# Performance work log

Measured on AMD Instinct MI355X. Metric: run time of the kernel, lower is better.

Reference implementation:

```python
import jax, jax.numpy as jnp
import numpy as np

NUM_HEADS = 16
ATTN_WINDOW = 128  # half-width; mask is |i-j| <= ATTN_WINDOW
EMBED_DIM = 1024


def setup_inputs() -> dict:
    key = jax.random.key(0)
    ks = jax.random.split(key, 9)
    B, S, D = 2, 2048, EMBED_DIM
    s = 1.0 / np.sqrt(D)
    inp = {
        "x": jax.random.normal(ks[0], (B, S, D), dtype=jnp.float32),
        "Wq": jax.random.normal(ks[1], (D, D), dtype=jnp.float32) * s,
        "bq": jnp.zeros((D,), dtype=jnp.float32),
        "Wk": jax.random.normal(ks[2], (D, D), dtype=jnp.float32) * s,
        "bk": jnp.zeros((D,), dtype=jnp.float32),
        "Wv": jax.random.normal(ks[3], (D, D), dtype=jnp.float32) * s,
        "bv": jnp.zeros((D,), dtype=jnp.float32),
        "Wo": jax.random.normal(ks[4], (D, D), dtype=jnp.float32) * s,
        "bo": jnp.zeros((D,), dtype=jnp.float32),
    }
    return inp


def reference(x, Wq, bq, Wk, bk, Wv, bv, Wo, bo):
    B, S, D = x.shape
    H = NUM_HEADS
    dh = D // H
    # projections (nn.Linear: x @ W^T + b)
    q = (x @ Wq.T + bq).reshape(B, S, H, dh).transpose(0, 2, 1, 3)  # [B,H,S,dh]
    k = (x @ Wk.T + bk).reshape(B, S, H, dh).transpose(0, 2, 1, 3)
    v = (x @ Wv.T + bv).reshape(B, S, H, dh).transpose(0, 2, 1, 3)
    scale = 1.0 / jnp.sqrt(jnp.asarray(dh, dtype=jnp.float32))
    scores = jnp.einsum("bhqd,bhkd->bhqk", q, k) * scale  # [B,H,S,S]
    # sliding-window band mask: allowed iff |i - j| <= ATTN_WINDOW
    idx = jnp.arange(S)
    band = jnp.abs(idx[:, None] - idx[None, :]) <= ATTN_WINDOW  # [S,S] bool
    scores = jnp.where(band[None, None], scores, -jnp.inf)
    attn = jax.nn.softmax(scores, axis=-1)  # each row has >=1 valid entry
    ctx = jnp.einsum("bhqk,bhkd->bhqd", attn, v)
    ctx = ctx.transpose(0, 2, 1, 3).reshape(B, S, D)
    out = ctx @ Wo.T + bo
    return out, attn
```

## Files before the change

kernel.cpp:

```cpp
#include <hip/hip_runtime.h>
#include <cstddef>

#define NB 2
#define NH 16
#define SQ 2048
#define DM 1024
#define DH 64
#define WN 128

using half8  = __attribute__((ext_vector_type(8))) _Float16;
using half4  = __attribute__((ext_vector_type(4))) _Float16;
using floatx4 = __attribute__((ext_vector_type(4))) float;

__device__ __forceinline__ void gl_lds16(const _Float16* g, _Float16* l) {
    __builtin_amdgcn_global_load_lds(
        (const __attribute__((address_space(1))) void*)g,
        (__attribute__((address_space(3))) void*)l, 16, 0, 0);
}

__global__ __launch_bounds__(256) void cvt1(const float* __restrict__ s,
                                            _Float16* __restrict__ d, int n8)
{
    int idx = blockIdx.x * 256 + threadIdx.x;
    if (idx < n8) {
        const float4 a = ((const float4*)s)[idx * 2];
        const float4 b = ((const float4*)s)[idx * 2 + 1];
        half8 h;
        h[0] = (_Float16)a.x; h[1] = (_Float16)a.y;
        h[2] = (_Float16)a.z; h[3] = (_Float16)a.w;
        h[4] = (_Float16)b.x; h[5] = (_Float16)b.y;
        h[6] = (_Float16)b.z; h[7] = (_Float16)b.w;
        ((half8*)d)[idx] = h;
    }
}

__global__ __launch_bounds__(256) void cvt4(
    const float* __restrict__ s0, const float* __restrict__ s1,
    const float* __restrict__ s2, const float* __restrict__ s3,
    _Float16* __restrict__ d0, _Float16* __restrict__ d1,
    _Float16* __restrict__ d2, _Float16* __restrict__ d3, int n8)
{
    const float* s = (blockIdx.y == 0) ? s0 : (blockIdx.y == 1) ? s1
                   : (blockIdx.y == 2) ? s2 : s3;
    _Float16*   d = (blockIdx.y == 0) ? d0 : (blockIdx.y == 1) ? d1
                   : (blockIdx.y == 2) ? d2 : d3;
    int idx = blockIdx.x * 256 + threadIdx.x;
    if (idx < n8) {
        const float4 a = ((const float4*)s)[idx * 2];
        const float4 b = ((const float4*)s)[idx * 2 + 1];
        half8 h;
        h[0] = (_Float16)a.x; h[1] = (_Float16)a.y;
        h[2] = (_Float16)a.z; h[3] = (_Float16)a.w;
        h[4] = (_Float16)b.x; h[5] = (_Float16)b.y;
        h[6] = (_Float16)b.z; h[7] = (_Float16)b.w;
        ((half8*)d)[idx] = h;
    }
}

template <int OUT_HALF>
__global__ __launch_bounds__(256) void gemm_h(
    const _Float16* __restrict__ A,
    const _Float16* __restrict__ W0, const _Float16* __restrict__ W1,
    const _Float16* __restrict__ W2,
    const float* __restrict__ b0, const float* __restrict__ b1,
    const float* __restrict__ b2,
    void* __restrict__ O0, void* __restrict__ O1, void* __restrict__ O2)
{
    constexpr int K = DM, N = DM, BK = 64;

    const _Float16* Wp = (blockIdx.z == 0) ? W0 : (blockIdx.z == 1) ? W1 : W2;
    const float*    bb = (blockIdx.z == 0) ? b0 : (blockIdx.z == 1) ? b1 : b2;
    void*           Op = (blockIdx.z == 0) ? O0 : (blockIdx.z == 1) ? O1 : O2;

    __shared__ _Float16 Asl[128 * BK];
    __shared__ _Float16 Bsl[128 * BK];

    const int tid  = threadIdx.x;
    const int lane = tid & 63;
    const int w    = tid >> 6;
    const int wm   = w & 1, wn = w >> 1;
    const int m0   = blockIdx.y * 128;
    const int n0   = blockIdx.x * 128;

    const int l8 = lane >> 3;
    const int lc = lane & 7;

    floatx4 acc[4][4];
#pragma unroll
    for (int t = 0; t < 4; ++t)
#pragma unroll
        for (int u = 0; u < 4; ++u) acc[t][u] = (floatx4){0.f, 0.f, 0.f, 0.f};

    for (int k0 = 0; k0 < K; k0 += BK) {
        __syncthreads();
#pragma unroll
        for (int i = 0; i < 4; ++i) {
            const int r  = w * 8 + l8 + i * 32;
            const int ca = lc ^ (r & 7);
            gl_lds16(A  + (size_t)(m0 + r) * K + k0 + ca * 8,
                     Asl + r * BK + lc * 8);
            gl_lds16(Wp + (size_t)(n0 + r) * K + k0 + ca * 8,
                     Bsl + r * BK + lc * 8);
        }
        __syncthreads();
#pragma unroll
        for (int kk = 0; kk < BK; kk += 32) {
            half8 af[4], bf[4];
            const int q = (kk >> 3) + (lane >> 4);
#pragma unroll
            for (int t = 0; t < 4; ++t) {
                const int ra = wm * 64 + t * 16 + (lane & 15);
                af[t] = *(const half8*)(Asl + ra * BK + ((q ^ (ra & 7)) << 3));
                const int rb = wn * 64 + t * 16 + (lane & 15);
                bf[t] = *(const half8*)(Bsl + rb * BK + ((q ^ (rb & 7)) << 3));
            }
#pragma unroll
            for (int t = 0; t < 4; ++t)
#pragma unroll
                for (int u = 0; u < 4; ++u)
                    acc[t][u] = __builtin_amdgcn_mfma_f32_16x16x32_f16(
                        af[t], bf[u], acc[t][u], 0, 0, 0);
        }
    }

    const int col0 = n0 + wn * 64 + (lane & 15);
    const int row0 = m0 + wm * 64 + ((lane >> 4) << 2);
#pragma unroll
    for (int u = 0; u < 4; ++u) {
        const int n = col0 + u * 16;
        const float bias = bb[n];
#pragma unroll
        for (int t = 0; t < 4; ++t) {
            const int m = row0 + t * 16;
#pragma unroll
            for (int r = 0; r < 4; ++r) {
                const float v = acc[t][u][r] + bias;
                if (OUT_HALF)
                    ((_Float16*)Op)[(size_t)(m + r) * N + n] = (_Float16)v;
                else
                    ((float*)Op)[(size_t)(m + r) * N + n] = v;
            }
        }
    }
}

__global__ __launch_bounds__(256, 3) void attn_mfma(
    const _Float16* __restrict__ Q, const _Float16* __restrict__ K,
    const _Float16* __restrict__ V, float* __restrict__ attn,
    _Float16* __restrict__ ctx)
{
    const int tid  = threadIdx.x;
    const int lane = tid & 63;
    const int w    = tid >> 6;
    const int h = blockIdx.y, b = blockIdx.z;
    const int i0 = blockIdx.x * 16;
    const int wo = i0 - WN;

    __shared__ __align__(16) char smem[54272];
    _Float16* KV = (_Float16*)smem;
    _Float16* Qs = (_Float16*)(smem + 34816);
    char*     Sb = smem + 36864;

    const int l8 = lane >> 3;
    const int lc = lane & 7;

#pragma unroll
    for (int i = 0; i < 8; ++i) {
        const int r  = w * 8 + l8 + i * 32;
        const int jg = wo + r;
        const int jc = jg < 0 ? 0 : (jg >= SQ ? SQ - 1 : jg);
        const int ca = lc ^ (r & 7);
        gl_lds16(K + ((size_t)(b * SQ + jc)) * DM + h * DH + ca * 8,
                 KV + r * 64 + lc * 8);
    }
    if (w < 2) {
        const int r  = 256 + w * 8 + l8;
        const int jg = wo + r;
        const int jc = jg >= SQ ? SQ - 1 : jg;
        const int ca = lc ^ (r & 7);
        gl_lds16(K + ((size_t)(b * SQ + jc)) * DM + h * DH + ca * 8,
                 KV + r * 64 + lc * 8);
    } else {
        const int r  = (w - 2) * 8 + l8;
        const int ca = lc ^ (r & 7);
        gl_lds16(Q + ((size_t)(b * SQ + i0 + r)) * DM + h * DH + ca * 8,
                 Qs + r * 64 + lc * 8);
    }

    half8 vr[9];
#pragma unroll
    for (int it = 0; it < 9; ++it) {
        const int idx = tid + 256 * it;
        const int j = idx >> 3, c8 = idx & 7;
        const int jg = wo + j;
        const int jc = jg < 0 ? 0 : (jg >= SQ ? SQ - 1 : jg);
        vr[it] = *(const half8*)(V + ((size_t)(b * SQ + jc)) * DM + h * DH + c8 * 8);
    }

    {
        const int a0 = wo > 0 ? wo : 0;
        const int b0 = (wo + 272 < SQ) ? (wo + 272) : SQ;
        const float4 z4 = make_float4(0.f, 0.f, 0.f, 0.f);
        float* abase = attn + ((size_t)(b * NH + h) * SQ + i0) * SQ;
        for (int idx = tid; idx < 16 * 512; idx += 256) {
            const int r  = idx >> 9;
            const int c4 = (idx & 511) << 2;
            if (c4 < a0 || c4 >= b0)
                *(float4*)(abase + (size_t)r * SQ + c4) = z4;
        }
    }

    __syncthreads();

    half8 af0, af1;
    {
        const int row = lane & 15;
        af0 = *(const half8*)(Qs + row * 64 + ((((lane >> 4))     ^ (row & 7)) << 3));
        af1 = *(const half8*)(Qs + row * 64 + (((4 + (lane >> 4)) ^ (row & 7)) << 3));
    }
    for (int t = w; t < 17; t += 4) {
        const int rb = t * 16 + (lane & 15);
        half8 bf0 = *(const half8*)(KV + rb * 64 + ((((lane >> 4))     ^ (rb & 7)) << 3));
        half8 bf1 = *(const half8*)(KV + rb * 64 + (((4 + (lane >> 4)) ^ (rb & 7)) << 3));
        floatx4 acc = (floatx4){0.f, 0.f, 0.f, 0.f};
        acc = __builtin_amdgcn_mfma_f32_16x16x32_f16(af0, bf0, acc, 0, 0, 0);
        acc = __builtin_amdgcn_mfma_f32_16x16x32_f16(af1, bf1, acc, 0, 0, 0);
        const int jloc = t * 16 + (lane & 15);
        const int jg   = wo + jloc;
        const bool inr = (jg >= 0) && (jg < SQ);
#pragma unroll
        for (int r = 0; r < 4; ++r) {
            const int q = ((lane >> 4) << 2) + r;
            const bool valid = ((unsigned)(jloc - q) <= 256u) && inr;
            ((float*)(Sb + q * 1088))[jloc] = valid ? acc[r] * 0.125f : -1e30f;
        }
    }
    __syncthreads();

#pragma unroll
    for (int it = 0; it < 9; ++it) {
        const int idx = tid + 256 * it;
        const int j = idx >> 3, c8 = idx & 7;
        const int jc3 = j >> 3, jl = j & 7;
#pragma unroll
        for (int e = 0; e < 8; ++e) {
            const int d  = c8 * 8 + e;
            const int f2 = (d + (d >> 3)) & 3;
            KV[d * 288 + ((jc3 ^ f2) << 3) + jl] = vr[it][e];
        }
    }

    for (int q = w; q < 16; q += 4) {
        const float* Srow = (const float*)(Sb + q * 1088);
        const float v0 = Srow[lane];
        const float v1 = Srow[lane + 64];
        const float v2 = Srow[lane + 128];
        const float v3 = Srow[lane + 192];
        const float v4 = (lane < 16) ? Srow[lane + 256] : -1e30f;
        float m = fmaxf(fmaxf(fmaxf(v0, v1), fmaxf(v2, v3)), v4);
        m = fmaxf(m, __shfl_xor(m, 32));
        m = fmaxf(m, __shfl_xor(m, 16));
        m = fmaxf(m, __shfl_xor(m, 8));
        m = fmaxf(m, __shfl_xor(m, 4));
        m = fmaxf(m, __shfl_xor(m, 2));
        m = fmaxf(m, __shfl_xor(m, 1));
        float e0 = __expf(v0 - m), e1 = __expf(v1 - m), e2 = __expf(v2 - m),
              e3 = __expf(v3 - m), e4 = __expf(v4 - m);
        float s = ((e0 + e1) + (e2 + e3)) + e4;
        s += __shfl_xor(s, 32); s += __shfl_xor(s, 16); s += __shfl_xor(s, 8);
        s += __shfl_xor(s, 4);  s += __shfl_xor(s, 2);  s += __shfl_xor(s, 1);
        const float inv = 1.0f / s;
        e0 *= inv; e1 *= inv; e2 *= inv; e3 *= inv; e4 *= inv;

        const int fq = (q + (q >> 3)) & 7;
        _Float16* Prow = (_Float16*)(Sb + q * 1088);
        Prow[((((lane      ) >> 3) ^ fq) << 3) + (lane & 7)] = (_Float16)e0;
        Prow[((((lane +  64) >> 3) ^ fq) << 3) + (lane & 7)] = (_Float16)e1;
        Prow[((((lane + 128) >> 3) ^ fq) << 3) + (lane & 7)] = (_Float16)e2;
        Prow[((((lane + 192) >> 3) ^ fq) << 3) + (lane & 7)] = (_Float16)e3;
        if (lane < 16) {
            Prow[((((lane + 256) >> 3) ^ fq) << 3) + (lane & 7)] = (_Float16)e4;
            Prow[((((lane + 272) >> 3) ^ fq) << 3) + (lane & 7)] =
                (_Float16)(0.0f * e4);
        }

        float* arow = attn + ((size_t)(b * NH + h) * SQ + i0 + q) * SQ;
        const int g0 = wo + lane;
        if ((unsigned)(g0      ) < (unsigned)SQ) arow[g0      ] = e0;
        if ((unsigned)(g0 +  64) < (unsigned)SQ) arow[g0 +  64] = e1;
        if ((unsigned)(g0 + 128) < (unsigned)SQ) arow[g0 + 128] = e2;
        if ((unsigned)(g0 + 192) < (unsigned)SQ) arow[g0 + 192] = e3;
        if (lane < 16 && (unsigned)(g0 + 256) < (unsigned)SQ) arow[g0 + 256] = e4;
    }
    __syncthreads();

    {
        const int rowp = lane & 15;
        const int fp = (rowp + (rowp >> 3)) & 7;
        const int rowv = w * 16 + (lane & 15);
        const int fv = (rowv + (rowv >> 3)) & 3;
        floatx4 acc = (floatx4){0.f, 0.f, 0.f, 0.f};
#pragma unroll
        for (int ks = 0; ks < 9; ++ks) {
            const int lch = ks * 4 + (lane >> 4);
            half8 ap = *(const half8*)(Sb + rowp * 1088 + ((lch ^ fp) << 4));
            half8 bp = *(const half8*)(KV + rowv * 288 + ((lch ^ fv) << 3));
            acc = __builtin_amdgcn_mfma_f32_16x16x32_f16(ap, bp, acc, 0, 0, 0);
        }
        const int dcol = w * 16 + (lane & 15);
#pragma unroll
        for (int r = 0; r < 4; ++r) {
            const int q = ((lane >> 4) << 2) + r;
            ctx[((size_t)(b * SQ + i0 + q)) * DM + h * DH + dcol] = (_Float16)acc[r];
        }
    }
}

extern "C" void kernel_launch(void* const* d_in, const int* in_sizes, int n_in,
                              void* d_out, int out_size, void* d_ws, size_t ws_size,
                              hipStream_t stream)
{
    const float* x  = (const float*)d_in[0];
    const float* Wq = (const float*)d_in[1];
    const float* bq = (const float*)d_in[2];
    const float* Wk = (const float*)d_in[3];
    const float* bk = (const float*)d_in[4];
    const float* Wv = (const float*)d_in[5];
    const float* bv = (const float*)d_in[6];
    const float* Wo = (const float*)d_in[7];
    const float* bo = (const float*)d_in[8];

    float* out  = (float*)d_out;
    float* attn = out + (size_t)NB * SQ * DM;

    const size_t tok = (size_t)NB * SQ * DM;
    const size_t wsz = (size_t)DM * DM;

    _Float16* xh   = (_Float16*)d_ws;
    _Float16* Wqh  = xh   + tok;
    _Float16* Wkh  = Wqh  + wsz;
    _Float16* Wvh  = Wkh  + wsz;
    _Float16* Woh  = Wvh  + wsz;
    _Float16* Qh   = Woh  + wsz;
    _Float16* Kh   = Qh   + tok;
    _Float16* Vh   = Kh   + tok;
    _Float16* ctxh = Vh   + tok;

    cvt1<<<dim3((int)(tok / 8 / 256)), dim3(256), 0, stream>>>(x, xh, (int)(tok / 8));
    cvt4<<<dim3((int)(wsz / 8 / 256), 4), dim3(256), 0, stream>>>(
        Wq, Wk, Wv, Wo, Wqh, Wkh, Wvh, Woh, (int)(wsz / 8));

    gemm_h<1><<<dim3(DM / 128, (NB * SQ) / 128, 3), dim3(256), 0, stream>>>(
        xh, Wqh, Wkh, Wvh, bq, bk, bv, Qh, Kh, Vh);

    attn_mfma<<<dim3(SQ / 16, NH, NB), dim3(256), 0, stream>>>(Qh, Kh, Vh, attn, ctxh);

    gemm_h<0><<<dim3(DM / 128, (NB * SQ) / 128, 1), dim3(256), 0, stream>>>(
        ctxh, Woh, Woh, Woh, bo, bo, bo, out, out, out);
}
```

Baseline: 666.4 us.

## Move attention-matrix zero fill into QKV projection GEMM mainloop

The attention kernel no longer zero-fills the out-of-band parts of the attn matrix. Instead the QKV GEMM zeroes the entire attn buffer, spreading the float4 stores across its K-loop iterations so they overlap with MFMA compute. The attention kernel then overwrites the band region. This writes the full matrix rather than only the masked part, adding store traffic in exchange for overlap, and correctness depends on the GEMM running before the attention kernel.

```diff
diff --git a/kernel.cpp b/kernel.cpp
--- a/kernel.cpp
+++ b/kernel.cpp
@@ -57,14 +57,15 @@
     }
 }
 
-template <int OUT_HALF>
+template <int OUT_HALF, int ZFILL>
 __global__ __launch_bounds__(256) void gemm_h(
     const _Float16* __restrict__ A,
     const _Float16* __restrict__ W0, const _Float16* __restrict__ W1,
     const _Float16* __restrict__ W2,
     const float* __restrict__ b0, const float* __restrict__ b1,
     const float* __restrict__ b2,
-    void* __restrict__ O0, void* __restrict__ O1, void* __restrict__ O2)
+    void* __restrict__ O0, void* __restrict__ O1, void* __restrict__ O2,
+    float* __restrict__ zf)
 {
     constexpr int K = DM, N = DM, BK = 64;
 
@@ -84,6 +85,12 @@
 
     const int l8 = lane >> 3;
     const int lc = lane & 7;
+
+    const size_t zbid    = (size_t)blockIdx.x
+                         + (size_t)gridDim.x * (blockIdx.y
+                         + (size_t)gridDim.y * blockIdx.z);
+    const size_t zstride = (size_t)gridDim.x * gridDim.y * gridDim.z * 256;
+    constexpr size_t ZTOT = (size_t)NB * NH * SQ * SQ / 4;
 
     floatx4 acc[4][4];
 #pragma unroll
@@ -101,6 +108,16 @@
                      Asl + r * BK + lc * 8);
             gl_lds16(Wp + (size_t)(n0 + r) * K + k0 + ca * 8,
                      Bsl + r * BK + lc * 8);
+        }
+        if (ZFILL) {
+            const int zstep = k0 >> 6;
+            const float4 z4 = make_float4(0.f, 0.f, 0.f, 0.f);
+#pragma unroll
+            for (int it = 0; it < 11; ++it) {
+                const size_t idx = ((size_t)zstep * 11 + it) * zstride
+                                 + zbid * 256 + tid;
+                if (idx < ZTOT) ((float4*)zf)[idx] = z4;
+            }
         }
         __syncthreads();
 #pragma unroll
@@ -195,19 +212,6 @@
         const int jg = wo + j;
         const int jc = jg < 0 ? 0 : (jg >= SQ ? SQ - 1 : jg);
         vr[it] = *(const half8*)(V + ((size_t)(b * SQ + jc)) * DM + h * DH + c8 * 8);
-    }
-
-    {
-        const int a0 = wo > 0 ? wo : 0;
-        const int b0 = (wo + 272 < SQ) ? (wo + 272) : SQ;
-        const float4 z4 = make_float4(0.f, 0.f, 0.f, 0.f);
-        float* abase = attn + ((size_t)(b * NH + h) * SQ + i0) * SQ;
-        for (int idx = tid; idx < 16 * 512; idx += 256) {
-            const int r  = idx >> 9;
-            const int c4 = (idx & 511) << 2;
-            if (c4 < a0 || c4 >= b0)
-                *(float4*)(abase + (size_t)r * SQ + c4) = z4;
-        }
     }
 
     __syncthreads();
@@ -350,11 +354,11 @@
     cvt4<<<dim3((int)(wsz / 8 / 256), 4), dim3(256), 0, stream>>>(
         Wq, Wk, Wv, Wo, Wqh, Wkh, Wvh, Woh, (int)(wsz / 8));
 
-    gemm_h<1><<<dim3(DM / 128, (NB * SQ) / 128, 3), dim3(256), 0, stream>>>(
-        xh, Wqh, Wkh, Wvh, bq, bk, bv, Qh, Kh, Vh);
+    gemm_h<1, 1><<<dim3(DM / 128, (NB * SQ) / 128, 3), dim3(256), 0, stream>>>(
+        xh, Wqh, Wkh, Wvh, bq, bk, bv, Qh, Kh, Vh, attn);
 
     attn_mfma<<<dim3(SQ / 16, NH, NB), dim3(256), 0, stream>>>(Qh, Kh, Vh, attn, ctxh);
 
-    gemm_h<0><<<dim3(DM / 128, (NB * SQ) / 128, 1), dim3(256), 0, stream>>>(
-        ctxh, Woh, Woh, Woh, bo, bo, bo, out, out, out);
-}
+    gemm_h<0, 0><<<dim3(DM / 128, (NB * SQ) / 128, 1), dim3(256), 0, stream>>>(
+        ctxh, Woh, Woh, Woh, bo, bo, bo, out, out, out, nullptr);
+}
```

Result: slower. 691.9 us (+3.8%).
